# Optimization experiments

Measured on AMD Instinct MI355X. Metric: run time of the kernel, lower is better.

Reference implementation:

```python
import jax, jax.numpy as jnp
import numpy as np

B, S, H = 32, 2048, 1024


def setup_inputs() -> dict:
    key = jax.random.key(0)
    k1, k2, k3, k4, k5, k6 = jax.random.split(key, 6)
    hidden = jax.random.normal(k1, (B, H), dtype=jnp.float32)
    encoder_outputs = jax.random.normal(k2, (B, S, H), dtype=jnp.float32)
    lengths = jax.random.randint(k3, (B,), 1, S + 1, dtype=jnp.int64)
    scale = 1.0 / np.sqrt(H)
    Wq = jax.random.normal(k4, (H, H), dtype=jnp.float32) * scale
    Wk = jax.random.normal(k5, (H, H), dtype=jnp.float32) * scale
    v = jax.random.uniform(k6, (H,), dtype=jnp.float32)  # torch.rand init
    return {"hidden": hidden, "encoder_outputs": encoder_outputs,
            "lengths": lengths, "Wq": Wq, "Wk": Wk, "v": v}


def reference(hidden, encoder_outputs, lengths, Wq, Wk, v):
    # query: (B, 1, H); nn.Linear(bias=False) applies x @ W.T
    query = (hidden @ Wq.T)[:, None, :]
    keys = jnp.einsum('bsh,kh->bsk', encoder_outputs, Wk)  # (B, S, H)
    energy = jnp.tanh(query + keys)                         # (B, S, H)
    attn = jnp.einsum('bsh,h->bs', energy, v)               # (B, S)
    seq = encoder_outputs.shape[1]
    mask = jnp.arange(seq)[None, :] < lengths[:, None]      # (B, S)
    attn = jnp.where(mask, attn, -jnp.inf)
    return jax.nn.softmax(attn, axis=1)
```

## Files before the change

kernel.cpp:

```cpp
#include <hip/hip_runtime.h>
#include <hip/hip_fp16.h>
#include <stdint.h>

#define B_SZ 32
#define S_SZ 2048
#define H_SZ 1024
#define M_SZ (B_SZ * S_SZ)

typedef _Float16 half8 __attribute__((ext_vector_type(8)));
typedef float floatx4 __attribute__((ext_vector_type(4)));

struct h4 { _Float16 x, y, z, w; };

__global__ __launch_bounds__(256) void convert_f32_to_f16(
    const float* __restrict__ in, h4* __restrict__ out, int n4) {
  int i = blockIdx.x * blockDim.x + threadIdx.x;
  int stride = gridDim.x * blockDim.x;
  const float4* in4 = (const float4*)in;
  for (; i < n4; i += stride) {
    float4 f = in4[i];
    h4 o;
    o.x = (_Float16)f.x; o.y = (_Float16)f.y;
    o.z = (_Float16)f.z; o.w = (_Float16)f.w;
    out[i] = o;
  }
}

__global__ __launch_bounds__(256) void query_kernel(
    const float* __restrict__ hidden, const float* __restrict__ Wq,
    float* __restrict__ q) {
  const int W = blockIdx.x * 4 + (threadIdx.x >> 6);
  const int lane = threadIdx.x & 63;
  const int b = W >> 10;
  const int n = W & 1023;
  const float4* hp = (const float4*)(hidden + (size_t)b * H_SZ);
  const float4* wp = (const float4*)(Wq + (size_t)n * H_SZ);
  float acc = 0.f;
  #pragma unroll
  for (int i = 0; i < 4; ++i) {
    float4 h = hp[lane + 64 * i];
    float4 w = wp[lane + 64 * i];
    acc = fmaf(h.x, w.x, acc);
    acc = fmaf(h.y, w.y, acc);
    acc = fmaf(h.z, w.z, acc);
    acc = fmaf(h.w, w.w, acc);
  }
  #pragma unroll
  for (int off = 32; off; off >>= 1) acc += __shfl_xor(acc, off);
  if (lane == 0) q[(size_t)b * H_SZ + n] = acc;
}

__device__ __forceinline__ void gl_lds16(const void* g, void* l) {
  __builtin_amdgcn_global_load_lds(
      (const __attribute__((address_space(1))) void*)g,
      (__attribute__((address_space(3))) void*)l,
      16, 0, 0);
}

__device__ __forceinline__ float fast_tanh(float x) {
  float ax = fabsf(x);
  float e = __expf(ax * -2.0f);
  float t = (1.0f - e) / (1.0f + e);
  return copysignf(t, x);
}

#define TILE 128
#define BK 32

__global__ __launch_bounds__(256) void fused_keys_kernel(
    const float* __restrict__ A,
    const _Float16* __restrict__ Bt,
    const float* __restrict__ q,
    const float* __restrict__ v,
    float* __restrict__ partial)
{
  __shared__ float    As[TILE * BK];
  __shared__ _Float16 Bs[TILE * BK];
  __shared__ float rowsum[TILE];
  __shared__ float q_l[TILE];
  __shared__ float v_l[TILE];

  const int tid  = threadIdx.x;
  const int w    = tid >> 6;
  const int lane = tid & 63;

  const int bm = ((blockIdx.x >> 6) << 3) | (blockIdx.x & 7);
  const int bn = (blockIdx.x >> 3) & 7;
  const int R0 = bm * TILE;
  const int C0 = bn * TILE;
  const int bidx = R0 >> 11;

  if (tid < TILE) {
    q_l[tid] = q[(size_t)bidx * H_SZ + C0 + tid];
    v_l[tid] = v[C0 + tid];
    rowsum[tid] = 0.f;
  }

  const int wm = w >> 1, wn = w & 1;
  const int cL = lane & 15, quad = lane >> 4;

  floatx4 acc[4][4];
  #pragma unroll
  for (int m = 0; m < 4; ++m)
    #pragma unroll
    for (int n = 0; n < 4; ++n)
      acc[m][n] = (floatx4){0.f, 0.f, 0.f, 0.f};

  const float* pA[4];
  #pragma unroll
  for (int i = 0; i < 4; ++i) {
    const int j = w * 4 + i;
    const int row = ((j >> 3) * 64) + (((j >> 1) & 3) * 16) + cL;
    const int kf  = quad * 8 + (j & 1) * 4;
    pA[i] = A + (size_t)(R0 + row) * H_SZ + kf;
  }
  const _Float16* pB[2];
  #pragma unroll
  for (int i = 0; i < 2; ++i) {
    const int j = w + 4 * i;
    const int row = ((j >> 2) * 64) + ((j & 3) * 16) + cL;
    pB[i] = Bt + (size_t)(C0 + row) * H_SZ + quad * 8;
  }

  for (int kt = 0; kt < H_SZ / BK; ++kt) {
    __syncthreads();
    #pragma unroll
    for (int i = 0; i < 4; ++i) {
      const int j = w * 4 + i;
      gl_lds16(pA[i], (char*)As + j * 1024);
      pA[i] += BK;
    }
    #pragma unroll
    for (int i = 0; i < 2; ++i) {
      const int j = w + 4 * i;
      gl_lds16(pB[i], (char*)Bs + j * 1024);
      pB[i] += BK;
    }
    __syncthreads();

    half8 af[4], bf[4];
    #pragma unroll
    for (int m = 0; m < 4; ++m) {
      float4 lo = *(const float4*)((const char*)As + wm * 8192 + m * 2048 + lane * 16);
      float4 hi = *(const float4*)((const char*)As + wm * 8192 + m * 2048 + 1024 + lane * 16);
      half8 a;
      a[0] = (_Float16)lo.x; a[1] = (_Float16)lo.y;
      a[2] = (_Float16)lo.z; a[3] = (_Float16)lo.w;
      a[4] = (_Float16)hi.x; a[5] = (_Float16)hi.y;
      a[6] = (_Float16)hi.z; a[7] = (_Float16)hi.w;
      af[m] = a;
    }
    #pragma unroll
    for (int n = 0; n < 4; ++n)
      bf[n] = *(const half8*)((const char*)Bs + wn * 4096 + n * 1024 + lane * 16);
    #pragma unroll
    for (int m = 0; m < 4; ++m)
      #pragma unroll
      for (int n = 0; n < 4; ++n)
        acc[m][n] = __builtin_amdgcn_mfma_f32_16x16x32_f16(af[m], bf[n], acc[m][n], 0, 0, 0);
  }

  float qv[4], vv[4];
  #pragma unroll
  for (int n = 0; n < 4; ++n) {
    const int col = wn * 64 + n * 16 + cL;
    qv[n] = q_l[col];
    vv[n] = v_l[col];
  }
  #pragma unroll
  for (int m = 0; m < 4; ++m) {
    #pragma unroll
    for (int r = 0; r < 4; ++r) {
      float s = 0.f;
      #pragma unroll
      for (int n = 0; n < 4; ++n)
        s += vv[n] * fast_tanh(qv[n] + acc[m][n][r]);
      s += __shfl_xor(s, 1);
      s += __shfl_xor(s, 2);
      s += __shfl_xor(s, 4);
      s += __shfl_xor(s, 8);
      if (cL == 0)
        atomicAdd(&rowsum[wm * 64 + m * 16 + quad * 4 + r], s);
    }
  }
  __syncthreads();
  if (tid < TILE)
    partial[(size_t)bn * M_SZ + R0 + tid] = rowsum[tid];
}

__global__ __launch_bounds__(256) void softmax_kernel(
    const float* __restrict__ partial, const int* __restrict__ lengths,
    float* __restrict__ out) {
  __shared__ float wred[4];
  __shared__ float wsum[4];
  const int b = blockIdx.x;
  const int tid = threadIdx.x;
  const int len = lengths[b];

  float lg[8];
  #pragma unroll
  for (int i = 0; i < 8; ++i) {
    const int s = tid + i * 256;
    const size_t row = (size_t)b * S_SZ + s;
    float l = 0.f;
    #pragma unroll
    for (int nt = 0; nt < 8; ++nt) l += partial[(size_t)nt * M_SZ + row];
    lg[i] = (s < len) ? l : -INFINITY;
  }

  float mx = lg[0];
  #pragma unroll
  for (int i = 1; i < 8; ++i) mx = fmaxf(mx, lg[i]);
  #pragma unroll
  for (int off = 32; off; off >>= 1) mx = fmaxf(mx, __shfl_xor(mx, off));
  if ((tid & 63) == 0) wred[tid >> 6] = mx;
  __syncthreads();
  mx = fmaxf(fmaxf(wred[0], wred[1]), fmaxf(wred[2], wred[3]));

  float pe[8];
  float sum = 0.f;
  #pragma unroll
  for (int i = 0; i < 8; ++i) {
    float e = (lg[i] == -INFINITY) ? 0.f : __expf(lg[i] - mx);
    pe[i] = e;
    sum += e;
  }
  #pragma unroll
  for (int off = 32; off; off >>= 1) sum += __shfl_xor(sum, off);
  if ((tid & 63) == 0) wsum[tid >> 6] = sum;
  __syncthreads();
  sum = wsum[0] + wsum[1] + wsum[2] + wsum[3];
  const float inv = 1.0f / sum;

  #pragma unroll
  for (int i = 0; i < 8; ++i) {
    const int s = tid + i * 256;
    out[(size_t)b * S_SZ + s] = pe[i] * inv;
  }
}

extern "C" void kernel_launch(void* const* d_in, const int* in_sizes, int n_in,
                              void* d_out, int out_size, void* d_ws, size_t ws_size,
                              hipStream_t stream) {
  const float* hidden  = (const float*)d_in[0];
  const float* enc     = (const float*)d_in[1];
  const int*   lengths = (const int*)d_in[2];
  const float* Wq      = (const float*)d_in[3];
  const float* Wk      = (const float*)d_in[4];
  const float* v       = (const float*)d_in[5];
  float* out = (float*)d_out;

  char* ws = (char*)d_ws;
  _Float16* B16     = (_Float16*)ws;
  float*    q       = (float*)(ws + 2097152);
  float*    partial = (float*)(ws + 2097152 + 131072);

  convert_f32_to_f16<<<1024, 256, 0, stream>>>(Wk, (h4*)B16, (H_SZ * H_SZ) / 4);
  query_kernel<<<8192, 256, 0, stream>>>(hidden, Wq, q);
  fused_keys_kernel<<<(M_SZ / TILE) * (H_SZ / TILE), 256, 0, stream>>>(enc, B16, q, v, partial);
  softmax_kernel<<<B_SZ, 256, 0, stream>>>(partial, lengths, out);
}
```

Measured before the change: 694.4 us.

## Pre-convert encoder outputs to fp16, double BK, fuse softmax via last-block counter

Adds a single prep kernel that converts the encoder outputs and Wk to fp16 and computes the query projection in one launch. The GEMM now loads fp16 A tiles directly with BK=64, removing per-iteration fp32-to-fp16 conversion and halving LDS traffic for A. The softmax is folded into the GEMM kernel: the last of 128 blocks per batch, detected with an atomic counter, performs it, which removes one launch. The trade-off is an extra 128 MB fp16 write and read of the encoder outputs against lower GEMM load and convert cost.

```diff
diff --git a/kernel.cpp b/kernel.cpp
--- a/kernel.cpp
+++ b/kernel.cpp
@@ -12,42 +12,60 @@
 
 struct h4 { _Float16 x, y, z, w; };
 
-__global__ __launch_bounds__(256) void convert_f32_to_f16(
-    const float* __restrict__ in, h4* __restrict__ out, int n4) {
-  int i = blockIdx.x * blockDim.x + threadIdx.x;
-  int stride = gridDim.x * blockDim.x;
-  const float4* in4 = (const float4*)in;
-  for (; i < n4; i += stride) {
-    float4 f = in4[i];
-    h4 o;
-    o.x = (_Float16)f.x; o.y = (_Float16)f.y;
-    o.z = (_Float16)f.z; o.w = (_Float16)f.w;
-    out[i] = o;
-  }
-}
-
-__global__ __launch_bounds__(256) void query_kernel(
+__global__ __launch_bounds__(256) void prep_kernel(
+    const float* __restrict__ enc, h4* __restrict__ A16,
+    const float* __restrict__ Wk, h4* __restrict__ B16,
     const float* __restrict__ hidden, const float* __restrict__ Wq,
-    float* __restrict__ q) {
-  const int W = blockIdx.x * 4 + (threadIdx.x >> 6);
-  const int lane = threadIdx.x & 63;
-  const int b = W >> 10;
-  const int n = W & 1023;
-  const float4* hp = (const float4*)(hidden + (size_t)b * H_SZ);
-  const float4* wp = (const float4*)(Wq + (size_t)n * H_SZ);
-  float acc = 0.f;
-  #pragma unroll
-  for (int i = 0; i < 4; ++i) {
-    float4 h = hp[lane + 64 * i];
-    float4 w = wp[lane + 64 * i];
-    acc = fmaf(h.x, w.x, acc);
-    acc = fmaf(h.y, w.y, acc);
-    acc = fmaf(h.z, w.z, acc);
-    acc = fmaf(h.w, w.w, acc);
-  }
-  #pragma unroll
-  for (int off = 32; off; off >>= 1) acc += __shfl_xor(acc, off);
-  if (lane == 0) q[(size_t)b * H_SZ + n] = acc;
+    float* __restrict__ q, unsigned* __restrict__ cnt)
+{
+  const int blk = blockIdx.x;
+  const int tid = threadIdx.x;
+  if (blk < 8192) {
+    int i = blk * 256 + tid;
+    const float4* in4 = (const float4*)enc;
+    #pragma unroll
+    for (int r = 0; r < 8; ++r) {
+      float4 f = in4[i];
+      h4 o;
+      o.x = (_Float16)f.x; o.y = (_Float16)f.y;
+      o.z = (_Float16)f.z; o.w = (_Float16)f.w;
+      A16[i] = o;
+      i += 8192 * 256;
+    }
+  } else if (blk < 8320) {
+    if (blk == 8192 && tid < B_SZ) cnt[tid] = 0u;
+    int i = (blk - 8192) * 256 + tid;
+    const float4* in4 = (const float4*)Wk;
+    #pragma unroll
+    for (int r = 0; r < 8; ++r) {
+      float4 f = in4[i];
+      h4 o;
+      o.x = (_Float16)f.x; o.y = (_Float16)f.y;
+      o.z = (_Float16)f.z; o.w = (_Float16)f.w;
+      B16[i] = o;
+      i += 128 * 256;
+    }
+  } else {
+    const int W = (blk - 8320) * 4 + (tid >> 6);
+    const int lane = tid & 63;
+    const int b = W >> 10;
+    const int n = W & 1023;
+    const float4* hp = (const float4*)(hidden + (size_t)b * H_SZ);
+    const float4* wp = (const float4*)(Wq + (size_t)n * H_SZ);
+    float acc = 0.f;
+    #pragma unroll
+    for (int i = 0; i < 4; ++i) {
+      float4 h = hp[lane + 64 * i];
+      float4 w = wp[lane + 64 * i];
+      acc = fmaf(h.x, w.x, acc);
+      acc = fmaf(h.y, w.y, acc);
+      acc = fmaf(h.z, w.z, acc);
+      acc = fmaf(h.w, w.w, acc);
+    }
+    #pragma unroll
+    for (int off = 32; off; off >>= 1) acc += __shfl_xor(acc, off);
+    if (lane == 0) q[(size_t)b * H_SZ + n] = acc;
+  }
 }
 
 __device__ __forceinline__ void gl_lds16(const void* g, void* l) {
@@ -65,20 +83,25 @@
 }
 
 #define TILE 128
-#define BK 32
+#define BK 64
 
 __global__ __launch_bounds__(256) void fused_keys_kernel(
-    const float* __restrict__ A,
+    const _Float16* __restrict__ A,
     const _Float16* __restrict__ Bt,
     const float* __restrict__ q,
     const float* __restrict__ v,
-    float* __restrict__ partial)
+    const int* __restrict__ lengths,
+    float* __restrict__ partial,
+    unsigned* __restrict__ cnt,
+    float* __restrict__ out)
 {
-  __shared__ float    As[TILE * BK];
+  __shared__ _Float16 As[TILE * BK];
   __shared__ _Float16 Bs[TILE * BK];
   __shared__ float rowsum[TILE];
   __shared__ float q_l[TILE];
   __shared__ float v_l[TILE];
+  __shared__ float red[8];
+  __shared__ unsigned last_s;
 
   const int tid  = threadIdx.x;
   const int w    = tid >> 6;
@@ -106,20 +129,15 @@
     for (int n = 0; n < 4; ++n)
       acc[m][n] = (floatx4){0.f, 0.f, 0.f, 0.f};
 
-  const float* pA[4];
+  const _Float16* pA[4];
+  const _Float16* pB[4];
   #pragma unroll
   for (int i = 0; i < 4; ++i) {
     const int j = w * 4 + i;
     const int row = ((j >> 3) * 64) + (((j >> 1) & 3) * 16) + cL;
-    const int kf  = quad * 8 + (j & 1) * 4;
-    pA[i] = A + (size_t)(R0 + row) * H_SZ + kf;
-  }
-  const _Float16* pB[2];
-  #pragma unroll
-  for (int i = 0; i < 2; ++i) {
-    const int j = w + 4 * i;
-    const int row = ((j >> 2) * 64) + ((j & 3) * 16) + cL;
-    pB[i] = Bt + (size_t)(C0 + row) * H_SZ + quad * 8;
+    const int k   = (j & 1) * 32 + quad * 8;
+    pA[i] = A  + (size_t)(R0 + row) * H_SZ + k;
+    pB[i] = Bt + (size_t)(C0 + row) * H_SZ + k;
   }
 
   for (int kt = 0; kt < H_SZ / BK; ++kt) {
@@ -128,36 +146,27 @@
     for (int i = 0; i < 4; ++i) {
       const int j = w * 4 + i;
       gl_lds16(pA[i], (char*)As + j * 1024);
+      gl_lds16(pB[i], (char*)Bs + j * 1024);
       pA[i] += BK;
-    }
-    #pragma unroll
-    for (int i = 0; i < 2; ++i) {
-      const int j = w + 4 * i;
-      gl_lds16(pB[i], (char*)Bs + j * 1024);
       pB[i] += BK;
     }
     __syncthreads();
 
-    half8 af[4], bf[4];
-    #pragma unroll
-    for (int m = 0; m < 4; ++m) {
-      float4 lo = *(const float4*)((const char*)As + wm * 8192 + m * 2048 + lane * 16);
-      float4 hi = *(const float4*)((const char*)As + wm * 8192 + m * 2048 + 1024 + lane * 16);
-      half8 a;
-      a[0] = (_Float16)lo.x; a[1] = (_Float16)lo.y;
-      a[2] = (_Float16)lo.z; a[3] = (_Float16)lo.w;
-      a[4] = (_Float16)hi.x; a[5] = (_Float16)hi.y;
-      a[6] = (_Float16)hi.z; a[7] = (_Float16)hi.w;
-      af[m] = a;
-    }
-    #pragma unroll
-    for (int n = 0; n < 4; ++n)
-      bf[n] = *(const half8*)((const char*)Bs + wn * 4096 + n * 1024 + lane * 16);
-    #pragma unroll
-    for (int m = 0; m < 4; ++m)
+    #pragma unroll
+    for (int ks = 0; ks < 2; ++ks) {
+      half8 af[4], bf[4];
+      #pragma unroll
+      for (int m = 0; m < 4; ++m)
+        af[m] = *(const half8*)((const char*)As + ((wm * 4 + m) * 2 + ks) * 1024 + lane * 16);
       #pragma unroll
       for (int n = 0; n < 4; ++n)
-        acc[m][n] = __builtin_amdgcn_mfma_f32_16x16x32_f16(af[m], bf[n], acc[m][n], 0, 0, 0);
+        bf[n] = *(const half8*)((const char*)Bs + ((wn * 4 + n) * 2 + ks) * 1024 + lane * 16);
+      #pragma unroll
+      for (int m = 0; m < 4; ++m)
+        #pragma unroll
+        for (int n = 0; n < 4; ++n)
+          acc[m][n] = __builtin_amdgcn_mfma_f32_16x16x32_f16(af[m], bf[n], acc[m][n], 0, 0, 0);
+    }
   }
 
   float qv[4], vv[4];
@@ -186,22 +195,21 @@
   __syncthreads();
   if (tid < TILE)
     partial[(size_t)bn * M_SZ + R0 + tid] = rowsum[tid];
-}
-
-__global__ __launch_bounds__(256) void softmax_kernel(
-    const float* __restrict__ partial, const int* __restrict__ lengths,
-    float* __restrict__ out) {
-  __shared__ float wred[4];
-  __shared__ float wsum[4];
-  const int b = blockIdx.x;
-  const int tid = threadIdx.x;
-  const int len = lengths[b];
-
+
+  __threadfence();
+  __syncthreads();
+  if (tid == 0)
+    last_s = (atomicAdd(&cnt[bidx], 1u) == 127u) ? 1u : 0u;
+  __syncthreads();
+  if (!last_s) return;
+  __threadfence();
+
+  const int len = lengths[bidx];
   float lg[8];
   #pragma unroll
   for (int i = 0; i < 8; ++i) {
     const int s = tid + i * 256;
-    const size_t row = (size_t)b * S_SZ + s;
+    const size_t row = (size_t)bidx * S_SZ + s;
     float l = 0.f;
     #pragma unroll
     for (int nt = 0; nt < 8; ++nt) l += partial[(size_t)nt * M_SZ + row];
@@ -213,9 +221,9 @@
   for (int i = 1; i < 8; ++i) mx = fmaxf(mx, lg[i]);
   #pragma unroll
   for (int off = 32; off; off >>= 1) mx = fmaxf(mx, __shfl_xor(mx, off));
-  if ((tid & 63) == 0) wred[tid >> 6] = mx;
-  __syncthreads();
-  mx = fmaxf(fmaxf(wred[0], wred[1]), fmaxf(wred[2], wred[3]));
+  if (lane == 0) red[w] = mx;
+  __syncthreads();
+  mx = fmaxf(fmaxf(red[0], red[1]), fmaxf(red[2], red[3]));
 
   float pe[8];
   float sum = 0.f;
@@ -227,15 +235,15 @@
   }
   #pragma unroll
   for (int off = 32; off; off >>= 1) sum += __shfl_xor(sum, off);
-  if ((tid & 63) == 0) wsum[tid >> 6] = sum;
-  __syncthreads();
-  sum = wsum[0] + wsum[1] + wsum[2] + wsum[3];
+  if (lane == 0) red[4 + w] = sum;
+  __syncthreads();
+  sum = red[4] + red[5] + red[6] + red[7];
   const float inv = 1.0f / sum;
 
   #pragma unroll
   for (int i = 0; i < 8; ++i) {
     const int s = tid + i * 256;
-    out[(size_t)b * S_SZ + s] = pe[i] * inv;
+    out[(size_t)bidx * S_SZ + s] = pe[i] * inv;
   }
 }
 
@@ -251,12 +259,14 @@
   float* out = (float*)d_out;
 
   char* ws = (char*)d_ws;
-  _Float16* B16     = (_Float16*)ws;
-  float*    q       = (float*)(ws + 2097152);
-  float*    partial = (float*)(ws + 2097152 + 131072);
-
-  convert_f32_to_f16<<<1024, 256, 0, stream>>>(Wk, (h4*)B16, (H_SZ * H_SZ) / 4);
-  query_kernel<<<8192, 256, 0, stream>>>(hidden, Wq, q);
-  fused_keys_kernel<<<(M_SZ / TILE) * (H_SZ / TILE), 256, 0, stream>>>(enc, B16, q, v, partial);
-  softmax_kernel<<<B_SZ, 256, 0, stream>>>(partial, lengths, out);
-}
+  _Float16* A16     = (_Float16*)ws;
+  _Float16* B16     = (_Float16*)(ws + 134217728);
+  float*    q       = (float*)(ws + 134217728 + 2097152);
+  float*    partial = (float*)(ws + 134217728 + 2097152 + 131072);
+  unsigned* cnt     = (unsigned*)(ws + 134217728 + 2097152 + 131072 + 2097152);
+
+  prep_kernel<<<16512, 256, 0, stream>>>(enc, (h4*)A16, Wk, (h4*)B16,
+                                         hidden, Wq, q, cnt);
+  fused_keys_kernel<<<(M_SZ / TILE) * (H_SZ / TILE), 256, 0, stream>>>(
+      A16, B16, q, v, lengths, partial, cnt, out);
+}
```

After: 937.6 us. 35.0% more time.
